# Kernel tuning notes

Hardware: AMD Instinct MI355X
Metric: run time of the kernel (lower is better)

The kernel has to match this reference:

```python
import jax, jax.numpy as jnp
from jax import lax
import numpy as np

THRESH = 0.5   # firing threshold of SpikeFunc
LENS = 0.5     # rectangular surrogate-gradient window half-width
DECAY = 0.2    # membrane potential decay (model_config['decay'])


@jax.custom_vjp
def spike(u):
    # Heaviside spike with rectangular surrogate gradient (STBP SpikeFunc)
    return (u > THRESH).astype(u.dtype)

def _spike_fwd(u):
    return spike(u), u

def _spike_bwd(u, g):
    return (g * (jnp.abs(u - THRESH) < LENS).astype(g.dtype),)

spike.defvjp(_spike_fwd, _spike_bwd)


def conv_s2(x, w, b):
    # 3x3 conv, stride 2, torch-style symmetric padding 1, NCHW
    y = lax.conv_general_dilated(x, w, (2, 2), ((1, 1), (1, 1)),
                                 dimension_numbers=("NCHW", "OIHW", "NCHW"))
    return y + b[None, :, None, None]


def setup_inputs() -> dict:
    key = jax.random.key(0)
    ks = jax.random.split(key, 7)
    bs, C, H, W, T = 32, 2, 128, 128, 20
    inp = {"input": jax.random.uniform(ks[0], (bs, C, H, W, T), jnp.float32)}
    wshapes = [(32, 2, 3, 3), (32, 32, 3, 3), (32, 32, 3, 3)]
    for i, s in enumerate(wshapes):
        fan_in = s[1] * s[2] * s[3]
        bound = float(1.0 / np.sqrt(fan_in))  # torch Conv2d default init range
        inp[f"w{i+1}"] = jax.random.uniform(ks[2*i+1], s, jnp.float32, -bound, bound)
        inp[f"b{i+1}"] = jax.random.uniform(ks[2*i+2], (s[0],), jnp.float32, -bound, bound)
    return inp


def reference(input, w1, b1, w2, b2, w3, b3):
    params = [(w1, b1), (w2, b2), (w3, b3)]
    bs = input.shape[0]
    # membrane / spike state shapes after each stride-2 conv: 128 -> 64 -> 32 -> 16
    state_shapes = [(bs, 32, 64, 64), (bs, 32, 32, 32), (bs, 32, 16, 16)]
    pots0 = tuple(jnp.zeros(s, input.dtype) for s in state_shapes)
    spks0 = tuple(jnp.zeros(s, input.dtype) for s in state_shapes)

    def step(carry, x_t):
        pots, spks = carry
        s = x_t  # spikes[0] = input[..., step]
        new_pots, new_spks = [], []
        for i, (w, b) in enumerate(params):
            # potential = potential*decay*(1-spike) + layer(x); spike = SpikeFunc(potential)
            u = pots[i] * DECAY * (1.0 - spks[i]) + conv_s2(s, w, b)
            sp = spike(u)
            new_pots.append(u)
            new_spks.append(sp)
            s = sp
        return (tuple(new_pots), tuple(new_spks)), s.reshape(bs, -1)

    xs = jnp.moveaxis(input, -1, 0)  # (T, bs, C, H, W)
    _, outs = lax.scan(step, (pots0, spks0), xs)  # outs: (T, bs, 8192)
    return jnp.moveaxis(outs, 0, -1)  # (bs, 8192, T)
```

## Files before the change

### kernel.cpp

```cpp
#include <hip/hip_runtime.h>
#include <cstdint>


#define DECAY 0.2f
#define TH 0.5f

typedef float v2f __attribute__((ext_vector_type(2)));

static __device__ __forceinline__ v2f pk_fma(v2f a, v2f b, v2f c) {
#if __has_builtin(__builtin_elementwise_fma)
    return __builtin_elementwise_fma(a, b, c);
#else
    v2f r;
    r.x = __builtin_fmaf(a.x, b.x, c.x);
    r.y = __builtin_fmaf(a.y, b.y, c.y);
    return r;
#endif
}

__global__ __launch_bounds__(256, 2)
void k1_conv(const float* __restrict__ in, const float* __restrict__ w1,
             const float* __restrict__ b1, uint8_t* __restrict__ sp1)
{
    __shared__ float P[20 * 816];

    const int tid = threadIdx.x;
    const int b   = blockIdx.x >> 6;
    const int row = blockIdx.x & 63;

    for (int idx = tid; idx < 3870; idx += 256) {
        int q = idx % 5, px = idx / 5;
        int iwl = px % 129, rest = px / 129;
        int ihl = rest % 3, ic = rest / 3;
        int ih = 2 * row - 1 + ihl;
        int iw = iwl - 1;
        float4 v = make_float4(0.f, 0.f, 0.f, 0.f);
        if (ih >= 0 && iw >= 0)
            v = *(const float4*)&in[(((size_t)(b * 2 + ic) * 128 + ih) * 128 + iw) * 20 + q * 4];
        int col = (iwl & 1) ? ((iwl - 1) >> 1) : (68 + (iwl >> 1));
        float* dst = &P[(ic * 3 + ihl) * 136 + col];
        int t0 = q * 4;
        dst[(t0 + 0) * 816] = v.x;
        dst[(t0 + 1) * 816] = v.y;
        dst[(t0 + 2) * 816] = v.z;
        dst[(t0 + 3) * 816] = v.w;
    }

    const int oc = tid >> 3;
    const int tw = tid & 7;

    float w[18];
    #pragma unroll
    for (int ic = 0; ic < 2; ic++)
        #pragma unroll
        for (int k9 = 0; k9 < 9; k9++)
            w[ic * 9 + k9] = w1[(oc * 2 + ic) * 9 + k9];
    const float bk = b1[oc];

    float pot[8];
    #pragma unroll
    for (int i = 0; i < 8; i++) pot[i] = 0.0f;

    __syncthreads();

    for (int t = 0; t < 20; t++) {
        float acc[8];
        #pragma unroll
        for (int i = 0; i < 8; i++) acc[i] = 0.0f;
        const float* Pt = &P[t * 816];
        #pragma unroll
        for (int ic = 0; ic < 2; ic++) {
            #pragma unroll
            for (int kh = 0; kh < 3; kh++) {
                const float* rowp = Pt + (ic * 3 + kh) * 136;
                float4 e0 = *(const float4*)&rowp[8 * tw];
                float4 e1 = *(const float4*)&rowp[8 * tw + 4];
                float4 o0 = *(const float4*)&rowp[68 + 8 * tw];
                float4 o1 = *(const float4*)&rowp[68 + 8 * tw + 4];
                float  o8 = rowp[68 + 8 * tw + 8];
                float wk0 = w[ic * 9 + kh * 3 + 0];
                float wk1 = w[ic * 9 + kh * 3 + 1];
                float wk2 = w[ic * 9 + kh * 3 + 2];
                acc[0] += wk0 * o0.x; acc[1] += wk0 * o0.y;
                acc[2] += wk0 * o0.z; acc[3] += wk0 * o0.w;
                acc[4] += wk0 * o1.x; acc[5] += wk0 * o1.y;
                acc[6] += wk0 * o1.z; acc[7] += wk0 * o1.w;
                acc[0] += wk1 * e0.x; acc[1] += wk1 * e0.y;
                acc[2] += wk1 * e0.z; acc[3] += wk1 * e0.w;
                acc[4] += wk1 * e1.x; acc[5] += wk1 * e1.y;
                acc[6] += wk1 * e1.z; acc[7] += wk1 * e1.w;
                acc[0] += wk2 * o0.y; acc[1] += wk2 * o0.z;
                acc[2] += wk2 * o0.w; acc[3] += wk2 * o1.x;
                acc[4] += wk2 * o1.y; acc[5] += wk2 * o1.z;
                acc[6] += wk2 * o1.w; acc[7] += wk2 * o8;
            }
        }
        uint32_t v = 0;
        #pragma unroll
        for (int j = 0; j < 8; j++) {
            float conv = acc[j] + bk;
            float pp = pot[j];
            float u = (pp > TH) ? conv : (pp * DECAY + conv);
            pot[j] = u;
            if (u > TH) v |= 1u << j;
        }
        sp1[(((size_t)(t * 32 + b) * 32 + oc) * 64 + row) * 8 + tw] = (uint8_t)v;
    }
}

__global__ __launch_bounds__(256, 3)
void k2a_conv(const uint8_t* __restrict__ sp1, const float* __restrict__ w2,
              float* __restrict__ S2)
{
    __shared__ float wl[9216];
    __shared__ unsigned long long B[544];

    const int tid  = threadIdx.x;
    const int bid  = blockIdx.x;
    const int t    = bid >> 7;
    const int rem  = bid & 127;
    const int b    = rem >> 2;
    const int band = rem & 3;
    const int oh0  = band << 3;

    for (int idx = tid; idx < 9216; idx += 256) {
        int oc = idx & 31, rest = idx >> 5;
        int ic = rest / 9, r9 = rest - ic * 9;
        wl[idx] = w2[(oc * 32 + ic) * 9 + r9];
    }
    const unsigned long long* sp1w = (const unsigned long long*)sp1;
    for (int idx = tid; idx < 544; idx += 256) {
        int ic = idx / 17, ihl = idx - ic * 17;
        int ih = 2 * oh0 - 1 + ihl;
        B[idx] = (ih >= 0) ? sp1w[((size_t)(t * 32 + b) * 32 + ic) * 64 + ih] : 0ull;
    }
    __syncthreads();

    const int oc0 = (tid >> 5) << 2;
    const int r   = (tid >> 2) & 7;
    const int owq = tid & 3;
    const int sshift = 16 * owq - 1;

    v2f acc[2][8];
    #pragma unroll
    for (int k = 0; k < 2; k++)
        #pragma unroll
        for (int j = 0; j < 8; j++) acc[k][j] = (v2f){0.0f, 0.0f};

    #pragma unroll 4
    for (int ic = 0; ic < 32; ic++) {
        #pragma unroll
        for (int kh = 0; kh < 3; kh++) {
            unsigned long long m = B[ic * 17 + 2 * r + kh];
            uint32_t bits = (sshift >= 0) ? (uint32_t)(m >> sshift)
                                          : (((uint32_t)m) << 1);
            float f[17];
            #pragma unroll
            for (int i = 0; i < 17; i++) f[i] = (float)((bits >> i) & 1u);
            const float* wb = &wl[(ic * 9 + kh * 3) * 32 + oc0];
            #pragma unroll
            for (int kw = 0; kw < 3; kw++) {
                v2f w01 = *(const v2f*)&wb[kw * 32];
                v2f w23 = *(const v2f*)&wb[kw * 32 + 2];
                #pragma unroll
                for (int j = 0; j < 8; j++) {
                    v2f fv = {f[2 * j + kw], f[2 * j + kw]};
                    acc[0][j] = pk_fma(w01, fv, acc[0][j]);
                    acc[1][j] = pk_fma(w23, fv, acc[1][j]);
                }
            }
        }
    }

    #pragma unroll
    for (int k = 0; k < 2; k++) {
        const int oc = oc0 + 2 * k;
        size_t base = ((size_t)(t * 32 + b) * 32 + oc) * 1024 + (oh0 + r) * 32 + owq * 8;
        float4 a0 = make_float4(acc[k][0].x, acc[k][1].x, acc[k][2].x, acc[k][3].x);
        float4 a1 = make_float4(acc[k][4].x, acc[k][5].x, acc[k][6].x, acc[k][7].x);
        float4 b0 = make_float4(acc[k][0].y, acc[k][1].y, acc[k][2].y, acc[k][3].y);
        float4 b1 = make_float4(acc[k][4].y, acc[k][5].y, acc[k][6].y, acc[k][7].y);
        *(float4*)&S2[base] = a0;
        *(float4*)&S2[base + 4] = a1;
        *(float4*)&S2[base + 1024] = b0;
        *(float4*)&S2[base + 1028] = b1;
    }
}

__global__ __launch_bounds__(256, 4)
void k2b_rec(const float* __restrict__ S2, const float* __restrict__ b2,
             uint8_t* __restrict__ sp2)
{
    const int bid = blockIdx.x;
    const int b   = bid >> 7;
    const int rem = bid & 127;
    const int oc  = rem >> 2;
    const int q   = rem & 3;
    const int tid = threadIdx.x;
    const int px  = q * 256 + tid;
    const float bk = b2[oc];
    uint32_t* sp2w = (uint32_t*)sp2;

    float sv[20];
    #pragma unroll
    for (int t = 0; t < 20; t++)
        sv[t] = S2[((size_t)(t * 32 + b) * 32 + oc) * 1024 + px];

    const int lane = tid & 63;
    float p = 0.0f;
    #pragma unroll
    for (int t = 0; t < 20; t++) {
        float conv = sv[t] + bk;
        float u = (p > TH) ? conv : (p * DECAY + conv);
        p = u;
        unsigned long long mk = __ballot(u > TH);
        if (lane == 0)
            sp2w[((size_t)(t * 32 + b) * 32 + oc) * 32 + (px >> 5)] = (uint32_t)mk;
        if (lane == 32)
            sp2w[((size_t)(t * 32 + b) * 32 + oc) * 32 + (px >> 5)] = (uint32_t)(mk >> 32);
    }
}

__global__ __launch_bounds__(256, 3)
void k3a_conv(const uint8_t* __restrict__ sp2, const float* __restrict__ w3,
              float* __restrict__ S3)
{
    __shared__ float wl[9216];
    __shared__ uint32_t Bs[1056];

    const int bid = blockIdx.x;
    const int t   = bid >> 5;
    const int b   = bid & 31;
    const int tid = threadIdx.x;
    const uint32_t* sp2w = (const uint32_t*)sp2;

    for (int idx = tid; idx < 9216; idx += 256) {
        int oc = idx & 31, rest = idx >> 5;
        int ic = rest / 9, r9 = rest - ic * 9;
        wl[idx] = w3[(oc * 32 + ic) * 9 + r9];
    }
    for (int idx = tid; idx < 1056; idx += 256) {
        int ic = idx / 33, ihl = idx - ic * 33;
        int ih = ihl - 1;
        Bs[idx] = (ih >= 0) ? sp2w[((size_t)(t * 32 + b) * 32 + ic) * 32 + ih] : 0u;
    }
    __syncthreads();

    const int oc0 = (tid >> 5) << 2;
    const int r   = (tid >> 1) & 15;
    const int owq = tid & 1;

    v2f acc[2][8];
    #pragma unroll
    for (int k = 0; k < 2; k++)
        #pragma unroll
        for (int j = 0; j < 8; j++) acc[k][j] = (v2f){0.0f, 0.0f};

    #pragma unroll 4
    for (int ic = 0; ic < 32; ic++) {
        #pragma unroll
        for (int kh = 0; kh < 3; kh++) {
            uint32_t m = Bs[ic * 33 + 2 * r + kh];
            uint32_t bits = owq ? (m >> 15) : (m << 1);
            float f[17];
            #pragma unroll
            for (int i = 0; i < 17; i++) f[i] = (float)((bits >> i) & 1u);
            const float* wb = &wl[(ic * 9 + kh * 3) * 32 + oc0];
            #pragma unroll
            for (int kw = 0; kw < 3; kw++) {
                v2f w01 = *(const v2f*)&wb[kw * 32];
                v2f w23 = *(const v2f*)&wb[kw * 32 + 2];
                #pragma unroll
                for (int j = 0; j < 8; j++) {
                    v2f fv = {f[2 * j + kw], f[2 * j + kw]};
                    acc[0][j] = pk_fma(w01, fv, acc[0][j]);
                    acc[1][j] = pk_fma(w23, fv, acc[1][j]);
                }
            }
        }
    }

    #pragma unroll
    for (int k = 0; k < 2; k++) {
        const int oc = oc0 + 2 * k;
        size_t base = ((size_t)(t * 32 + b) * 32 + oc) * 256 + r * 16 + owq * 8;
        float4 a0 = make_float4(acc[k][0].x, acc[k][1].x, acc[k][2].x, acc[k][3].x);
        float4 a1 = make_float4(acc[k][4].x, acc[k][5].x, acc[k][6].x, acc[k][7].x);
        float4 b0 = make_float4(acc[k][0].y, acc[k][1].y, acc[k][2].y, acc[k][3].y);
        float4 b1 = make_float4(acc[k][4].y, acc[k][5].y, acc[k][6].y, acc[k][7].y);
        *(float4*)&S3[base] = a0;
        *(float4*)&S3[base + 4] = a1;
        *(float4*)&S3[base + 256] = b0;
        *(float4*)&S3[base + 260] = b1;
    }
}

__global__ __launch_bounds__(256, 4)
void k3b_rec(const float* __restrict__ S3, const float* __restrict__ b3,
             float* __restrict__ out)
{
    const int b  = blockIdx.x >> 5;
    const int oc = blockIdx.x & 31;
    const int tid = threadIdx.x;
    const float bk = b3[oc];

    float p = 0.0f;
    uint32_t om = 0u;
    for (int t = 0; t < 20; t++) {
        float s = S3[((size_t)(t * 32 + b) * 32 + oc) * 256 + tid];
        float conv = s + bk;
        float u = (p > TH) ? conv : (p * DECAY + conv);
        p = u;
        if (u > TH) om |= 1u << t;
    }
    float* dst = &out[((size_t)b * 8192 + (oc << 8) + tid) * 20];
    #pragma unroll
    for (int qq = 0; qq < 5; qq++) {
        float4 v;
        v.x = ((om >> (qq * 4 + 0)) & 1u) ? 1.0f : 0.0f;
        v.y = ((om >> (qq * 4 + 1)) & 1u) ? 1.0f : 0.0f;
        v.z = ((om >> (qq * 4 + 2)) & 1u) ? 1.0f : 0.0f;
        v.w = ((om >> (qq * 4 + 3)) & 1u) ? 1.0f : 0.0f;
        *(float4*)&dst[qq * 4] = v;
    }
}

__global__ __launch_bounds__(256, 2)
void k2_conv(const uint8_t* __restrict__ sp1, const float* __restrict__ w2,
             const float* __restrict__ b2, uint8_t* __restrict__ sp2)
{
    __shared__ float wl[9216];
    __shared__ unsigned long long B[544];

    const int tid  = threadIdx.x;
    const int b    = blockIdx.x >> 4;
    const int tile = blockIdx.x & 15;
    const int oh0  = (tile >> 2) << 3;
    const int ow0  = (tile & 3) << 3;

    for (int idx = tid; idx < 9216; idx += 256) {
        int oc = idx & 31, rest = idx >> 5;
        int ic = rest / 9, r9 = rest - ic * 9;
        wl[idx] = w2[(oc * 32 + ic) * 9 + r9];
    }

    const unsigned long long* sp1w = (const unsigned long long*)sp1;
    int w0i = tid, w1i = 256 + tid, w2i = 512 + tid;
    int ic0s = w0i / 17, ih0 = 2 * oh0 - 1 + (w0i - ic0s * 17);
    int ic1s = w1i / 17, ih1 = 2 * oh0 - 1 + (w1i - ic1s * 17);
    int ic2s = w2i / 17, ih2 = 2 * oh0 - 1 + (w2i - ic2s * 17);
    const size_t base0 = (size_t)(b * 32 + ic0s) * 64 + ih0;
    const size_t base1 = (size_t)(b * 32 + ic1s) * 64 + ih1;
    const size_t base2 = (size_t)(b * 32 + ic2s) * 64 + ih2;
    const bool v0ok = (ih0 >= 0), v1ok = (ih1 >= 0), v2ok = (tid < 32) && (ih2 >= 0);

    unsigned long long v0 = v0ok ? sp1w[base0] : 0ull;
    unsigned long long v1 = v1ok ? sp1w[base1] : 0ull;
    unsigned long long v2 = v2ok ? sp1w[base2] : 0ull;

    const int oc0 = (tid >> 5) << 2;
    const int sl  = tid & 31;
    const int r   = sl >> 2;
    const int owp = sl & 3, owl = owp << 1;
    const int sshift = 2 * (ow0 + owl) - 1;

    const float4 bias = *(const float4*)&b2[oc0];
    float pot[8];
    #pragma unroll
    for (int i = 0; i < 8; i++) pot[i] = 0.0f;

    for (int t = 0; t < 20; t++) {
        __syncthreads();
        B[tid] = v0;
        B[256 + tid] = v1;
        if (tid < 32) B[512 + tid] = v2;
        __syncthreads();
        if (t < 19) {
            size_t ts = (size_t)(t + 1) * 65536;
            v0 = v0ok ? sp1w[ts + base0] : 0ull;
            v1 = v1ok ? sp1w[ts + base1] : 0ull;
            v2 = v2ok ? sp1w[ts + base2] : 0ull;
        }

        float acc[8];
        #pragma unroll
        for (int i = 0; i < 8; i++) acc[i] = 0.0f;
        const unsigned long long* Bp = &B[2 * r];
        #pragma unroll 4
        for (int ic = 0; ic < 32; ic++) {
            #pragma unroll
            for (int kh = 0; kh < 3; kh++) {
                unsigned long long m = Bp[ic * 17 + kh];
                uint32_t bits = (sshift >= 0) ? (uint32_t)(m >> sshift)
                                              : (((uint32_t)m) << 1);
                float f0 = (float)(bits & 1u);
                float f1 = (float)((bits >> 1) & 1u);
                float f2 = (float)((bits >> 2) & 1u);
                float f3 = (float)((bits >> 3) & 1u);
                float f4 = (float)((bits >> 4) & 1u);
                const float* wb = &wl[(ic * 9 + kh * 3) * 32 + oc0];
                float4 wk0 = *(const float4*)(wb);
                float4 wk1 = *(const float4*)(wb + 32);
                float4 wk2 = *(const float4*)(wb + 64);
                acc[0] += wk0.x * f0;  acc[1] += wk0.x * f2;
                acc[2] += wk0.y * f0;  acc[3] += wk0.y * f2;
                acc[4] += wk0.z * f0;  acc[5] += wk0.z * f2;
                acc[6] += wk0.w * f0;  acc[7] += wk0.w * f2;
                acc[0] += wk1.x * f1;  acc[1] += wk1.x * f3;
                acc[2] += wk1.y * f1;  acc[3] += wk1.y * f3;
                acc[4] += wk1.z * f1;  acc[5] += wk1.z * f3;
                acc[6] += wk1.w * f1;  acc[7] += wk1.w * f3;
                acc[0] += wk2.x * f2;  acc[1] += wk2.x * f4;
                acc[2] += wk2.y * f2;  acc[3] += wk2.y * f4;
                acc[4] += wk2.z * f2;  acc[5] += wk2.z * f4;
                acc[6] += wk2.w * f2;  acc[7] += wk2.w * f4;
            }
        }

        uint32_t p = 0;
        #pragma unroll
        for (int k = 0; k < 4; k++) {
            float bkk = ((const float*)&bias)[k];
            uint32_t v = 0;
            #pragma unroll
            for (int w = 0; w < 2; w++) {
                float conv = acc[k * 2 + w] + bkk;
                float pp = pot[k * 2 + w];
                float u = (pp > TH) ? conv : (pp * DECAY + conv);
                pot[k * 2 + w] = u;
                if (u > TH) v |= 1u << (owl + w);
            }
            p |= v << (8 * k);
        }
        p |= __shfl_xor((int)p, 1);
        p |= __shfl_xor((int)p, 2);
        if (owp == 0) {
            #pragma unroll
            for (int k = 0; k < 4; k++)
                sp2[(((size_t)(t * 32 + b) * 32 + (oc0 + k)) * 32 + (oh0 + r)) * 4 + (ow0 >> 3)]
                    = (uint8_t)(p >> (8 * k));
        }
    }
}

__global__ __launch_bounds__(256, 3)
void k3_fused(const uint8_t* __restrict__ sp2, const float* __restrict__ w3,
              const float* __restrict__ b3, float* __restrict__ out)
{
    __shared__ float wl[9216];
    __shared__ float P[8 * 9 * 18];

    const int tid  = threadIdx.x;
    const int b    = blockIdx.x >> 3;
    const int tile = blockIdx.x & 7;
    const int oh0  = (tile >> 1) << 2;
    const int ow0  = (tile & 1) << 3;

    for (int idx = tid; idx < 9216; idx += 256) {
        int oc = idx & 31, rest = idx >> 5;
        int ic = rest / 9, r9 = rest - ic * 9;
        wl[idx] = w3[(oc * 32 + ic) * 9 + r9];
    }

    const int ocg = tid >> 4, oc0 = ocg << 1;
    const int sl = tid & 15, r = sl >> 2, owp = sl & 3, owl = owp << 1;
    const float2 bias = *(const float2*)&b3[oc0];
    float pot[4];
    uint32_t om[4];
    #pragma unroll
    for (int i = 0; i < 4; i++) { pot[i] = 0.0f; om[i] = 0u; }

    for (int t = 0; t < 20; t++) {
        float acc[4];
        #pragma unroll
        for (int i = 0; i < 4; i++) acc[i] = 0.0f;
        for (int cc = 0; cc < 4; cc++) {
            __syncthreads();
            if (tid < 72) {
                int ic = tid / 9, ihl = tid - ic * 9;
                int ih = 2 * oh0 - 1 + ihl;
                uint32_t rowb = 0u;
                if (ih >= 0)
                    rowb = *(const uint32_t*)
                           &sp2[(((size_t)(t * 32 + b) * 32 + (cc * 8 + ic)) * 32 + ih) * 4];
                float* dst = &P[(ic * 9 + ihl) * 18];
                #pragma unroll
                for (int iwl = 0; iwl < 17; iwl++) {
                    int iw = 2 * ow0 - 1 + iwl;
                    int col = (iwl & 1) ? ((iwl - 1) >> 1) : (8 + (iwl >> 1));
                    dst[col] = (iw >= 0 && ((rowb >> iw) & 1u)) ? 1.0f : 0.0f;
                }
            }
            __syncthreads();
            #pragma unroll
            for (int ic = 0; ic < 8; ic++) {
                #pragma unroll
                for (int kh = 0; kh < 3; kh++) {
                    const float* row = &P[(ic * 9 + 2 * r + kh) * 18];
                    float eA = row[owl],     eB = row[owl + 1];
                    float oA = row[8 + owl], oB = row[9 + owl], oC = row[10 + owl];
                    const float* wb = &wl[((cc * 8 + ic) * 9 + kh * 3) * 32 + oc0];
                    float2 w0  = *(const float2*)(wb);
                    float2 w1v = *(const float2*)(wb + 32);
                    float2 w2v = *(const float2*)(wb + 64);
                    acc[0] += w0.x * oA;  acc[1] += w0.x * oB;
                    acc[2] += w0.y * oA;  acc[3] += w0.y * oB;
                    acc[0] += w1v.x * eA; acc[1] += w1v.x * eB;
                    acc[2] += w1v.y * eA; acc[3] += w1v.y * eB;
                    acc[0] += w2v.x * oB; acc[1] += w2v.x * oC;
                    acc[2] += w2v.y * oB; acc[3] += w2v.y * oC;
                }
            }
        }
        #pragma unroll
        for (int k = 0; k < 2; k++) {
            float bk = (k == 0) ? bias.x : bias.y;
            #pragma unroll
            for (int w = 0; w < 2; w++) {
                float conv = acc[k * 2 + w] + bk;
                float pp = pot[k * 2 + w];
                float u = (pp > TH) ? conv : (pp * DECAY + conv);
                pot[k * 2 + w] = u;
                if (u > TH) om[k * 2 + w] |= 1u << t;
            }
        }
    }

    #pragma unroll
    for (int k = 0; k < 2; k++) {
        #pragma unroll
        for (int w = 0; w < 2; w++) {
            int oc = oc0 + k;
            int oh = oh0 + r, ow = ow0 + owl + w;
            int i = (oc << 8) + (oh << 4) + ow;
            float* dst = &out[((size_t)b * 8192 + i) * 20];
            uint32_t m = om[k * 2 + w];
            #pragma unroll
            for (int qq = 0; qq < 5; qq++) {
                float4 v;
                v.x = ((m >> (qq * 4 + 0)) & 1u) ? 1.0f : 0.0f;
                v.y = ((m >> (qq * 4 + 1)) & 1u) ? 1.0f : 0.0f;
                v.z = ((m >> (qq * 4 + 2)) & 1u) ? 1.0f : 0.0f;
                v.w = ((m >> (qq * 4 + 3)) & 1u) ? 1.0f : 0.0f;
                *(float4*)&dst[qq * 4] = v;
            }
        }
    }
}

extern "C" void kernel_launch(void* const* d_in, const int* in_sizes, int n_in,
                              void* d_out, int out_size, void* d_ws, size_t ws_size,
                              hipStream_t stream)
{
    (void)in_sizes; (void)n_in; (void)out_size;
    const float* in = (const float*)d_in[0];
    const float* w1 = (const float*)d_in[1];
    const float* b1 = (const float*)d_in[2];
    const float* w2 = (const float*)d_in[3];
    const float* b2 = (const float*)d_in[4];
    const float* w3 = (const float*)d_in[5];
    const float* b3 = (const float*)d_in[6];

    const size_t SP1_BYTES = (size_t)20 * 32 * 32 * 64 * 8;
    const size_t SP2_BYTES = (size_t)20 * 32 * 32 * 32 * 4;
    const size_t S2_BYTES  = (size_t)20 * 32 * 32 * 1024 * 4;
    const size_t S3_BYTES  = (size_t)20 * 32 * 32 * 256 * 4;

    uint8_t* base = (uint8_t*)d_ws;
    const bool full = ws_size >= SP1_BYTES + SP2_BYTES + S2_BYTES;
    const bool mid  = ws_size >= S3_BYTES + SP2_BYTES;

    if (full) {
        uint8_t* sp1 = base;
        uint8_t* sp2 = base + SP1_BYTES;
        float*   S2  = (float*)(base + SP1_BYTES + SP2_BYTES);
        float*   S3  = (float*)(base + SP1_BYTES + SP2_BYTES);
        k1_conv<<<32 * 64, 256, 0, stream>>>(in, w1, b1, sp1);
        k2a_conv<<<20 * 32 * 4, 256, 0, stream>>>(sp1, w2, S2);
        k2b_rec<<<32 * 32 * 4, 256, 0, stream>>>(S2, b2, sp2);
        k3a_conv<<<20 * 32, 256, 0, stream>>>(sp2, w3, S3);
        k3b_rec<<<32 * 32, 256, 0, stream>>>(S3, b3, (float*)d_out);
    } else if (mid) {
        uint8_t* sp1 = base;
        float*   S3  = (float*)base;
        uint8_t* sp2 = base + S3_BYTES;
        k1_conv<<<32 * 64, 256, 0, stream>>>(in, w1, b1, sp1);
        k2_conv<<<32 * 16, 256, 0, stream>>>(sp1, w2, b2, sp2);
        k3a_conv<<<20 * 32, 256, 0, stream>>>(sp2, w3, S3);
        k3b_rec<<<32 * 32, 256, 0, stream>>>(S3, b3, (float*)d_out);
    } else {
        uint8_t* sp1 = base;
        uint8_t* sp2 = base + SP1_BYTES;
        k1_conv<<<32 * 64, 256, 0, stream>>>(in, w1, b1, sp1);
        k2_conv<<<32 * 16, 256, 0, stream>>>(sp1, w2, b2, sp2);
        k3_fused<<<32 * 8, 256, 0, stream>>>(sp2, w3, b3, (float*)d_out);
    }
}
```

Baseline: 532.9 us.

## Feed conv weights as wave-uniform scalar operands instead of LDS

Adds a weight-transpose prep kernel so each wave handles a group of eight output channels and reads its weights as wave-uniform values from global memory. Packed FMAs then take the weights through SGPR operands via inline asm, which removes the 36KB LDS weight tile and its staging loop. The k2a tiling is also reworked (16-row bands, four oc pairs per thread) and occupancy hints are raised. The inline asm forces scalar weight loads and adds an extra launch. In the full path w2t is placed in the sp2 buffer before k2b overwrites it, and w3t sits after the aliased S2/S3 region, both of which are fragile.

New measurement: 485.1 us. -9.0%, faster.

```diff
diff --git a/kernel.cpp b/kernel.cpp
--- a/kernel.cpp
+++ b/kernel.cpp
@@ -7,15 +7,23 @@
 
 typedef float v2f __attribute__((ext_vector_type(2)));
 
-static __device__ __forceinline__ v2f pk_fma(v2f a, v2f b, v2f c) {
-#if __has_builtin(__builtin_elementwise_fma)
-    return __builtin_elementwise_fma(a, b, c);
-#else
-    v2f r;
-    r.x = __builtin_fmaf(a.x, b.x, c.x);
-    r.y = __builtin_fmaf(a.y, b.y, c.y);
-    return r;
-#endif
+static __device__ __forceinline__ v2f pk_fma_sv(v2f w, v2f f, v2f acc) {
+    asm("v_pk_fma_f32 %0, %1, %2, %0" : "+v"(acc) : "s"(w), "v"(f));
+    return acc;
+}
+
+__global__ __launch_bounds__(256, 4)
+void wt_prep(const float* __restrict__ w, float* __restrict__ wt)
+{
+    int idx = blockIdx.x * 256 + threadIdx.x;
+    if (idx < 9216) {
+        int ocl = idx & 7;
+        int r9  = (idx >> 3) % 9;
+        int icg = idx / 72;
+        int ic  = icg & 31;
+        int ocg = icg >> 5;
+        wt[idx] = w[((ocg * 8 + ocl) * 32 + ic) * 9 + r9];
+    }
 }
 
 __global__ __launch_bounds__(256, 2)
@@ -108,82 +116,79 @@
     }
 }
 
-__global__ __launch_bounds__(256, 3)
-void k2a_conv(const uint8_t* __restrict__ sp1, const float* __restrict__ w2,
+__global__ __launch_bounds__(256, 4)
+void k2a_conv(const uint8_t* __restrict__ sp1, const float* __restrict__ w2t,
               float* __restrict__ S2)
 {
-    __shared__ float wl[9216];
-    __shared__ unsigned long long B[544];
+    __shared__ unsigned long long B[1056];
 
     const int tid  = threadIdx.x;
     const int bid  = blockIdx.x;
-    const int t    = bid >> 7;
-    const int rem  = bid & 127;
-    const int b    = rem >> 2;
-    const int band = rem & 3;
-    const int oh0  = band << 3;
-
-    for (int idx = tid; idx < 9216; idx += 256) {
-        int oc = idx & 31, rest = idx >> 5;
-        int ic = rest / 9, r9 = rest - ic * 9;
-        wl[idx] = w2[(oc * 32 + ic) * 9 + r9];
-    }
+    const int t    = bid >> 6;
+    const int rem  = bid & 63;
+    const int b    = rem >> 1;
+    const int band = rem & 1;
+    const int oh0  = band << 4;
+
     const unsigned long long* sp1w = (const unsigned long long*)sp1;
-    for (int idx = tid; idx < 544; idx += 256) {
-        int ic = idx / 17, ihl = idx - ic * 17;
+    for (int idx = tid; idx < 1056; idx += 256) {
+        int ic = idx / 33, ihl = idx - ic * 33;
         int ih = 2 * oh0 - 1 + ihl;
         B[idx] = (ih >= 0) ? sp1w[((size_t)(t * 32 + b) * 32 + ic) * 64 + ih] : 0ull;
     }
     __syncthreads();
 
-    const int oc0 = (tid >> 5) << 2;
-    const int r   = (tid >> 2) & 7;
-    const int owq = tid & 3;
-    const int sshift = 16 * owq - 1;
-
-    v2f acc[2][8];
-    #pragma unroll
-    for (int k = 0; k < 2; k++)
+    const int ocgu = __builtin_amdgcn_readfirstlane(tid >> 6);
+    const int lane = tid & 63;
+    const int r    = lane >> 2;
+    const int owq  = lane & 3;
+    const float* wt = w2t + ocgu * 2304;
+
+    v2f acc[4][8];
+    #pragma unroll
+    for (int k = 0; k < 4; k++)
         #pragma unroll
         for (int j = 0; j < 8; j++) acc[k][j] = (v2f){0.0f, 0.0f};
 
-    #pragma unroll 4
+    #pragma unroll 2
     for (int ic = 0; ic < 32; ic++) {
         #pragma unroll
         for (int kh = 0; kh < 3; kh++) {
-            unsigned long long m = B[ic * 17 + 2 * r + kh];
-            uint32_t bits = (sshift >= 0) ? (uint32_t)(m >> sshift)
-                                          : (((uint32_t)m) << 1);
-            float f[17];
-            #pragma unroll
-            for (int i = 0; i < 17; i++) f[i] = (float)((bits >> i) & 1u);
-            const float* wb = &wl[(ic * 9 + kh * 3) * 32 + oc0];
+            unsigned long long m = B[ic * 33 + 2 * r + kh];
+            uint32_t bits = owq ? (uint32_t)(m >> (16 * owq - 1))
+                                : (((uint32_t)m) << 1);
+            v2f fp[17];
+            #pragma unroll
+            for (int i = 0; i < 17; i++) {
+                float fv = (float)((bits >> i) & 1u);
+                fp[i] = (v2f){fv, fv};
+            }
+            const float* wp = wt + (ic * 9 + kh * 3) * 8;
             #pragma unroll
             for (int kw = 0; kw < 3; kw++) {
-                v2f w01 = *(const v2f*)&wb[kw * 32];
-                v2f w23 = *(const v2f*)&wb[kw * 32 + 2];
                 #pragma unroll
-                for (int j = 0; j < 8; j++) {
-                    v2f fv = {f[2 * j + kw], f[2 * j + kw]};
-                    acc[0][j] = pk_fma(w01, fv, acc[0][j]);
-                    acc[1][j] = pk_fma(w23, fv, acc[1][j]);
+                for (int ocp = 0; ocp < 4; ocp++) {
+                    v2f wv = *(const v2f*)(wp + kw * 8 + 2 * ocp);
+                    #pragma unroll
+                    for (int j = 0; j < 8; j++)
+                        acc[ocp][j] = pk_fma_sv(wv, fp[2 * j + kw], acc[ocp][j]);
                 }
             }
         }
     }
 
     #pragma unroll
-    for (int k = 0; k < 2; k++) {
-        const int oc = oc0 + 2 * k;
+    for (int ocp = 0; ocp < 4; ocp++) {
+        const int oc = ocgu * 8 + 2 * ocp;
         size_t base = ((size_t)(t * 32 + b) * 32 + oc) * 1024 + (oh0 + r) * 32 + owq * 8;
-        float4 a0 = make_float4(acc[k][0].x, acc[k][1].x, acc[k][2].x, acc[k][3].x);
-        float4 a1 = make_float4(acc[k][4].x, acc[k][5].x, acc[k][6].x, acc[k][7].x);
-        float4 b0 = make_float4(acc[k][0].y, acc[k][1].y, acc[k][2].y, acc[k][3].y);
-        float4 b1 = make_float4(acc[k][4].y, acc[k][5].y, acc[k][6].y, acc[k][7].y);
-        *(float4*)&S2[base] = a0;
-        *(float4*)&S2[base + 4] = a1;
-        *(float4*)&S2[base + 1024] = b0;
-        *(float4*)&S2[base + 1028] = b1;
+        float4 x0 = make_float4(acc[ocp][0].x, acc[ocp][1].x, acc[ocp][2].x, acc[ocp][3].x);
+        float4 x1 = make_float4(acc[ocp][4].x, acc[ocp][5].x, acc[ocp][6].x, acc[ocp][7].x);
+        float4 y0 = make_float4(acc[ocp][0].y, acc[ocp][1].y, acc[ocp][2].y, acc[ocp][3].y);
+        float4 y1 = make_float4(acc[ocp][4].y, acc[ocp][5].y, acc[ocp][6].y, acc[ocp][7].y);
+        *(float4*)&S2[base] = x0;
+        *(float4*)&S2[base + 4] = x1;
+        *(float4*)&S2[base + 1024] = y0;
+        *(float4*)&S2[base + 1028] = y1;
     }
 }
 
@@ -221,11 +226,10 @@
     }
 }
 
-__global__ __launch_bounds__(256, 3)
-void k3a_conv(const uint8_t* __restrict__ sp2, const float* __restrict__ w3,
+__global__ __launch_bounds__(256, 4)
+void k3a_conv(const uint8_t* __restrict__ sp2, const float* __restrict__ w3t,
               float* __restrict__ S3)
 {
-    __shared__ float wl[9216];
     __shared__ uint32_t Bs[1056];
 
     const int bid = blockIdx.x;
@@ -234,11 +238,6 @@
     const int tid = threadIdx.x;
     const uint32_t* sp2w = (const uint32_t*)sp2;
 
-    for (int idx = tid; idx < 9216; idx += 256) {
-        int oc = idx & 31, rest = idx >> 5;
-        int ic = rest / 9, r9 = rest - ic * 9;
-        wl[idx] = w3[(oc * 32 + ic) * 9 + r9];
-    }
     for (int idx = tid; idx < 1056; idx += 256) {
         int ic = idx / 33, ihl = idx - ic * 33;
         int ih = ihl - 1;
@@ -246,52 +245,52 @@
     }
     __syncthreads();
 
-    const int oc0 = (tid >> 5) << 2;
-    const int r   = (tid >> 1) & 15;
-    const int owq = tid & 1;
-
-    v2f acc[2][8];
-    #pragma unroll
-    for (int k = 0; k < 2; k++)
-        #pragma unroll
-        for (int j = 0; j < 8; j++) acc[k][j] = (v2f){0.0f, 0.0f};
-
-    #pragma unroll 4
+    const int ocgu = __builtin_amdgcn_readfirstlane(tid >> 6);
+    const int lane = tid & 63;
+    const int r    = lane >> 2;
+    const int owq  = lane & 3;
+    const float* wt = w3t + ocgu * 2304;
+
+    v2f acc[4][4];
+    #pragma unroll
+    for (int k = 0; k < 4; k++)
+        #pragma unroll
+        for (int j = 0; j < 4; j++) acc[k][j] = (v2f){0.0f, 0.0f};
+
+    #pragma unroll 2
     for (int ic = 0; ic < 32; ic++) {
         #pragma unroll
         for (int kh = 0; kh < 3; kh++) {
             uint32_t m = Bs[ic * 33 + 2 * r + kh];
-            uint32_t bits = owq ? (m >> 15) : (m << 1);
-            float f[17];
-            #pragma unroll
-            for (int i = 0; i < 17; i++) f[i] = (float)((bits >> i) & 1u);
-            const float* wb = &wl[(ic * 9 + kh * 3) * 32 + oc0];
+            uint32_t bits = owq ? (m >> (8 * owq - 1)) : (m << 1);
+            v2f fp[9];
+            #pragma unroll
+            for (int i = 0; i < 9; i++) {
+                float fv = (float)((bits >> i) & 1u);
+                fp[i] = (v2f){fv, fv};
+            }
+            const float* wp = wt + (ic * 9 + kh * 3) * 8;
             #pragma unroll
             for (int kw = 0; kw < 3; kw++) {
-                v2f w01 = *(const v2f*)&wb[kw * 32];
-                v2f w23 = *(const v2f*)&wb[kw * 32 + 2];
                 #pragma unroll
-                for (int j = 0; j < 8; j++) {
-                    v2f fv = {f[2 * j + kw], f[2 * j + kw]};
-                    acc[0][j] = pk_fma(w01, fv, acc[0][j]);
-                    acc[1][j] = pk_fma(w23, fv, acc[1][j]);
+                for (int ocp = 0; ocp < 4; ocp++) {
+                    v2f wv = *(const v2f*)(wp + kw * 8 + 2 * ocp);
+                    #pragma unroll
+                    for (int j = 0; j < 4; j++)
+                        acc[ocp][j] = pk_fma_sv(wv, fp[2 * j + kw], acc[ocp][j]);
                 }
             }
         }
     }
 
     #pragma unroll
-    for (int k = 0; k < 2; k++) {
-        const int oc = oc0 + 2 * k;
-        size_t base = ((size_t)(t * 32 + b) * 32 + oc) * 256 + r * 16 + owq * 8;
-        float4 a0 = make_float4(acc[k][0].x, acc[k][1].x, acc[k][2].x, acc[k][3].x);
-        float4 a1 = make_float4(acc[k][4].x, acc[k][5].x, acc[k][6].x, acc[k][7].x);
-        float4 b0 = make_float4(acc[k][0].y, acc[k][1].y, acc[k][2].y, acc[k][3].y);
-        float4 b1 = make_float4(acc[k][4].y, acc[k][5].y, acc[k][6].y, acc[k][7].y);
-        *(float4*)&S3[base] = a0;
-        *(float4*)&S3[base + 4] = a1;
-        *(float4*)&S3[base + 256] = b0;
-        *(float4*)&S3[base + 260] = b1;
+    for (int ocp = 0; ocp < 4; ocp++) {
+        const int oc = ocgu * 8 + 2 * ocp;
+        size_t base = ((size_t)(t * 32 + b) * 32 + oc) * 256 + r * 16 + owq * 4;
+        float4 x0 = make_float4(acc[ocp][0].x, acc[ocp][1].x, acc[ocp][2].x, acc[ocp][3].x);
+        float4 y0 = make_float4(acc[ocp][0].y, acc[ocp][1].y, acc[ocp][2].y, acc[ocp][3].y);
+        *(float4*)&S3[base] = x0;
+        *(float4*)&S3[base + 256] = y0;
     }
 }
 
@@ -565,28 +564,35 @@
     const size_t SP2_BYTES = (size_t)20 * 32 * 32 * 32 * 4;
     const size_t S2_BYTES  = (size_t)20 * 32 * 32 * 1024 * 4;
     const size_t S3_BYTES  = (size_t)20 * 32 * 32 * 256 * 4;
+    const size_t WT_BYTES  = (size_t)9216 * 4;
 
     uint8_t* base = (uint8_t*)d_ws;
     const bool full = ws_size >= SP1_BYTES + SP2_BYTES + S2_BYTES;
-    const bool mid  = ws_size >= S3_BYTES + SP2_BYTES;
+    const bool mid  = ws_size >= S3_BYTES + SP2_BYTES + WT_BYTES;
 
     if (full) {
         uint8_t* sp1 = base;
         uint8_t* sp2 = base + SP1_BYTES;
         float*   S2  = (float*)(base + SP1_BYTES + SP2_BYTES);
         float*   S3  = (float*)(base + SP1_BYTES + SP2_BYTES);
+        float*   w2t = (float*)sp2;
+        float*   w3t = (float*)(base + SP1_BYTES + SP2_BYTES + S3_BYTES);
         k1_conv<<<32 * 64, 256, 0, stream>>>(in, w1, b1, sp1);
-        k2a_conv<<<20 * 32 * 4, 256, 0, stream>>>(sp1, w2, S2);
+        wt_prep<<<36, 256, 0, stream>>>(w2, w2t);
+        k2a_conv<<<20 * 32 * 2, 256, 0, stream>>>(sp1, w2t, S2);
         k2b_rec<<<32 * 32 * 4, 256, 0, stream>>>(S2, b2, sp2);
-        k3a_conv<<<20 * 32, 256, 0, stream>>>(sp2, w3, S3);
+        wt_prep<<<36, 256, 0, stream>>>(w3, w3t);
+        k3a_conv<<<20 * 32, 256, 0, stream>>>(sp2, w3t, S3);
         k3b_rec<<<32 * 32, 256, 0, stream>>>(S3, b3, (float*)d_out);
     } else if (mid) {
         uint8_t* sp1 = base;
         float*   S3  = (float*)base;
         uint8_t* sp2 = base + S3_BYTES;
+        float*   w3t = (float*)(base + S3_BYTES + SP2_BYTES);
         k1_conv<<<32 * 64, 256, 0, stream>>>(in, w1, b1, sp1);
         k2_conv<<<32 * 16, 256, 0, stream>>>(sp1, w2, b2, sp2);
-        k3a_conv<<<20 * 32, 256, 0, stream>>>(sp2, w3, S3);
+        wt_prep<<<36, 256, 0, stream>>>(w3, w3t);
+        k3a_conv<<<20 * 32, 256, 0, stream>>>(sp2, w3t, S3);
         k3b_rec<<<32 * 32, 256, 0, stream>>>(S3, b3, (float*)d_out);
     } else {
         uint8_t* sp1 = base;
```
